# Optimization experiments

Measured on AMD Instinct MI355X. Metric: run time of the kernel, lower is better.

## Reference

```python
import jax, jax.numpy as jnp
import numpy as np

DIM = 512; HEADS = 8; DH = 64; INNER = HEADS * DH
GAMMA = 0.01; LREG = 1e-3
QB = 16; NS = 512


def _ln(x, g, b):
    mu = x.mean(-1, keepdims=True)
    var = jnp.var(x, axis=-1, keepdims=True)  # biased, matches torch LayerNorm
    return (x - mu) / jnp.sqrt(var + 1e-5) * g + b


def _std(x):
    return jnp.std(x, ddof=1)  # torch.std default is unbiased


def setup_inputs() -> dict:
    key = jax.random.key(0)
    ks = jax.random.split(key, 10)
    sc = lambda k, shape: (jax.random.normal(k, shape, jnp.float32) * 0.05)
    return {
        "q": jax.random.normal(ks[0], (QB, NS, DIM), jnp.float32),
        "k": jax.random.normal(ks[1], (QB, NS, DIM), jnp.float32),
        "v": jax.random.normal(ks[2], (QB, NS, DIM), jnp.float32),
        "ln1_g": jnp.ones((DIM,), jnp.float32),
        "ln1_b": jnp.zeros((DIM,), jnp.float32),
        "W_in": sc(ks[3], (DIM, INNER)),
        "wp_w1": sc(ks[4], (2 * DH, 2 * DH)),
        "wp_b1": jnp.zeros((2 * DH,), jnp.float32),
        "wp_ln_g": jnp.ones((2 * DH,), jnp.float32),
        "wp_ln_b": jnp.zeros((2 * DH,), jnp.float32),
        "wp_w2": sc(ks[5], (2 * DH, DH)),
        "wp_b2": jnp.zeros((DH,), jnp.float32),
        "wp_w3": sc(ks[6], (DH, 3)),
        "wp_b3": jnp.zeros((3,), jnp.float32),
        "weight_temp": jnp.array([0.5], jnp.float32),
        "W_out": sc(ks[7], (INNER, DIM)),
        "b_out": jnp.zeros((DIM,), jnp.float32),
    }


def _forward(q, k, v, ln1_g, ln1_b, W_in, wp_w1, wp_b1, wp_ln_g, wp_ln_b,
             wp_w2, wp_b2, wp_w3, wp_b3, weight_temp, W_out, b_out):
    eps = 1e-6

    def proj(t):  # LayerNorm -> Linear(no bias) -> [h, q, n, d]
        y = _ln(t, ln1_g, ln1_b) @ W_in
        Qb, Nb, _ = y.shape
        return y.reshape(Qb, Nb, HEADS, DH).transpose(2, 0, 1, 3)

    f_q, f_k, f_v = proj(q), proj(k), proj(v)
    m = f_k.shape[2]

    # --- cosine distance component ---
    dots_raw = jnp.einsum('hqnd,hqmd->hqnm', f_q, f_k)
    n1 = jnp.linalg.norm(f_q, axis=-1, keepdims=True) + eps          # [h,q,n,1]
    n2 = jnp.linalg.norm(f_k, axis=-1)[:, :, None, :] + eps          # [h,q,1,m]
    cosine_sim = jnp.clip(dots_raw / (n1 * n2), -0.9, 0.9)

    # --- regularized covariance component ---
    fkc = f_k - f_k.mean(axis=2, keepdims=True)   # center keys over n
    fqc = f_q - f_q.mean(axis=-1, keepdims=True)  # center queries over d
    cov = jnp.einsum('hqnd,hqmd->hqnm', fqc, fkc) / (DH ** 0.5 + 1e-6)
    cov = jnp.clip((LREG / max(m, 1)) * cov, -10.0, 10.0)

    # --- margin-based variance component (eval: adaptive_gamma = gamma) ---
    fqn = f_q / jnp.maximum(jnp.linalg.norm(f_q, axis=-1, keepdims=True), 1e-6)
    fkn = f_k / jnp.maximum(jnp.linalg.norm(f_k, axis=-1, keepdims=True), 1e-6)
    cs = jnp.clip(jnp.einsum('hqnd,hqmd->hqnm', fqn, fkn), -0.9, 0.9)
    margin = jnp.clip(GAMMA - cs, 0.0, 5.0)
    var_comp = jnp.broadcast_to(margin.mean(-1, keepdims=True), cs.shape)

    # --- dynamic per-head mixture weights ---
    feat = jnp.concatenate([f_q.mean((1, 2)), f_k.mean((1, 2))], axis=-1)  # [h, 2d]
    x = jax.nn.relu(_ln(feat @ wp_w1 + wp_b1, wp_ln_g, wp_ln_b))
    x = jax.nn.relu(x @ wp_w2 + wp_b2)
    wlog = jax.nn.softmax(x @ wp_w3 + wp_b3, axis=-1)  # predictor ends in Softmax
    wt = jnp.clip(weight_temp, 0.1, 2.0)
    w = jax.nn.softmax(wlog / wt, axis=-1)             # second softmax over temp
    w = jnp.clip(w, 0.05, 0.8)
    w = w / w.sum(-1, keepdims=True)
    cos_w = w[:, 0].reshape(HEADS, 1, 1, 1)
    cov_w = w[:, 1].reshape(HEADS, 1, 1, 1)
    var_w = w[:, 2].reshape(HEADS, 1, 1, 1)

    sg = jax.lax.stop_gradient  # norms are .detach()'d in torch
    dots = (cos_w * (cosine_sim / (sg(_std(cosine_sim)) + 1e-6))
            + cov_w * (cov / (sg(_std(cov)) + 1e-6) * 0.5)
            + var_w * (var_comp / (sg(_std(var_comp)) + 1e-6) * 0.5))

    ds = _std(dots)
    temp = jnp.where(ds < 1e-4, jnp.float32(0.1),
                     jnp.where(ds < 0.01, jnp.float32(0.3), 0.5 + ds))
    temp = jnp.clip(temp, 0.1, 3.0)

    attn = jax.nn.softmax(dots / temp, axis=-1)
    out = jnp.einsum('hqnm,hqmd->hqnd', attn, f_v)
    out = out.transpose(1, 2, 0, 3).reshape(q.shape[0], q.shape[1], INNER)
    return out @ W_out + b_out


def reference(q, k, v, ln1_g, ln1_b, W_in, wp_w1, wp_b1, wp_ln_g, wp_ln_b,
              wp_w2, wp_b2, wp_w3, wp_b3, weight_temp, W_out, b_out):
    return _forward(q, k, v, ln1_g, ln1_b, W_in, wp_w1, wp_b1, wp_ln_g,
                    wp_ln_b, wp_w2, wp_b2, wp_w3, wp_b3, weight_temp,
                    W_out, b_out)
```

## Files before the change

### kernel.cpp

```cpp
#include <hip/hip_runtime.h>
#include <math.h>

#define H 8
#define NS 512
#define D 64

typedef __bf16 bf16x8 __attribute__((ext_vector_type(8)));
typedef float f32x4 __attribute__((ext_vector_type(4)));
typedef short s16x8 __attribute__((ext_vector_type(8)));
typedef short s16x4 __attribute__((ext_vector_type(4)));

#define CS2 ((1e-3f/512.f)/(8.f+1e-6f))
#define LOG2E 1.4426950408889634

static __device__ __forceinline__ f32x4 mfma16(bf16x8 a, bf16x8 b, f32x4 c){
  return __builtin_amdgcn_mfma_f32_16x16x32_bf16(a,b,c,0,0,0);
}
static __device__ __forceinline__ float b2f(unsigned short s){
  union { unsigned u; float f; } v; v.u = ((unsigned)s)<<16; return v.f;
}
static __device__ __forceinline__ unsigned short f2b(float f){
  union { float f; unsigned u; } v; v.f = f;
  unsigned r = v.u + 0x7FFFu + ((v.u>>16)&1u);
  return (unsigned short)(r>>16);
}
static __device__ __forceinline__ float wred64(float v){
  #pragma unroll
  for(int m=32; m>0; m>>=1) v += __shfl_xor(v, m, 64);
  return v;
}

constexpr size_t OFF_XNB = 0;
constexpr size_t OFF_FQB = 6291456;
constexpr size_t OFF_FKB = 8388608;
constexpr size_t OFF_FVB = 10485760;
constexpr size_t OFF_FVT = 12582912;
constexpr size_t OFF_WT  = 14680064;
constexpr size_t OFF_WOH = 14811136;
constexpr size_t OFF_WOL = 14942208;
constexpr size_t OFF_OHH = 15073280;
constexpr size_t OFF_OHL = 17170432;
constexpr size_t OFF_ARR = 19267584;
constexpr size_t OFF_MKB = OFF_ARR + 9*65536;
constexpr size_t OFF_SMK = OFF_MKB + 8192;
constexpr size_t OFF_COEF= OFF_SMK + 128;
constexpr size_t OFF_DBL = OFF_COEF + 32;
constexpr size_t NDBL    = 72 + 1024;

__global__ __launch_bounds__(256) void k_tw(const float* __restrict__ W, unsigned short* __restrict__ WT,
    double* __restrict__ dbl){
  int bx = blockIdx.x; int kt = bx>>3, nt = bx&7;
  int t = threadIdx.x;
  if(bx==0){
    for(int i=t;i<(int)NDBL;i+=256) dbl[i]=0.0;
  }
  __shared__ float tile[64][65];
  #pragma unroll
  for(int i=0;i<4;i++){
    int row = (t>>4) + i*16; int col = (t&15)*4;
    float4 v = *(const float4*)(W + (size_t)(kt*64+row)*512 + nt*64 + col);
    tile[row][col]=v.x; tile[row][col+1]=v.y; tile[row][col+2]=v.z; tile[row][col+3]=v.w;
  }
  __syncthreads();
  #pragma unroll
  for(int i=0;i<4;i++){
    int n = (t>>4) + i*16; int ck = (t&15)*4;
    s16x4 o;
    #pragma unroll
    for(int j=0;j<4;j++) o[j] = (short)f2b(tile[ck+j][n]);
    *(s16x4*)(WT + (size_t)(nt*64+n)*512 + kt*64 + ck) = o;
  }
}

__global__ __launch_bounds__(256) void k_two(const float* __restrict__ W,
    unsigned short* __restrict__ WTh, unsigned short* __restrict__ WTl){
  int bx = blockIdx.x; int kt = bx>>3, nt = bx&7;
  __shared__ float tile[64][65];
  int t = threadIdx.x;
  #pragma unroll
  for(int i=0;i<4;i++){
    int row = (t>>4) + i*16; int col = (t&15)*4;
    float4 v = *(const float4*)(W + (size_t)(kt*64+row)*512 + nt*64 + col);
    tile[row][col]=v.x; tile[row][col+1]=v.y; tile[row][col+2]=v.z; tile[row][col+3]=v.w;
  }
  __syncthreads();
  #pragma unroll
  for(int i=0;i<4;i++){
    int n = (t>>4) + i*16; int ck = (t&15)*4;
    s16x4 oh_, ol_;
    #pragma unroll
    for(int j=0;j<4;j++){
      float x = tile[ck+j][n];
      unsigned short hi = f2b(x);
      oh_[j] = (short)hi;
      ol_[j] = (short)f2b(x - b2f(hi));
    }
    *(s16x4*)(WTh + (size_t)(nt*64+n)*512 + kt*64 + ck) = oh_;
    *(s16x4*)(WTl + (size_t)(nt*64+n)*512 + kt*64 + ck) = ol_;
  }
}

__global__ __launch_bounds__(256) void k_ln(const float* __restrict__ q,
    const float* __restrict__ k, const float* __restrict__ v,
    const float* __restrict__ g, const float* __restrict__ b,
    unsigned short* __restrict__ xnb){
  int row = blockIdx.x*4 + (threadIdx.x>>6); int t = threadIdx.x & 63;
  const float* src = (row < 8192) ? q : ((row < 16384) ? k : v);
  int r = row & 8191;
  const float4* sp = (const float4*)(src + (size_t)r*512);
  float4 v1 = sp[t*2], v2 = sp[t*2+1];
  float s  = v1.x+v1.y+v1.z+v1.w + v2.x+v2.y+v2.z+v2.w;
  float ss = v1.x*v1.x+v1.y*v1.y+v1.z*v1.z+v1.w*v1.w
           + v2.x*v2.x+v2.y*v2.y+v2.z*v2.z+v2.w*v2.w;
  s = wred64(s); ss = wred64(ss);
  float mu = s*(1.f/512.f);
  float var = ss*(1.f/512.f) - mu*mu;
  float rstd = rsqrtf(var + 1e-5f);
  const float4* gp = (const float4*)g; const float4* bp = (const float4*)b;
  float4 g1 = gp[t*2], g2 = gp[t*2+1], b1 = bp[t*2], b2 = bp[t*2+1];
  s16x8 o;
  o[0]=(short)f2b((v1.x-mu)*rstd*g1.x+b1.x); o[1]=(short)f2b((v1.y-mu)*rstd*g1.y+b1.y);
  o[2]=(short)f2b((v1.z-mu)*rstd*g1.z+b1.z); o[3]=(short)f2b((v1.w-mu)*rstd*g1.w+b1.w);
  o[4]=(short)f2b((v2.x-mu)*rstd*g2.x+b2.x); o[5]=(short)f2b((v2.y-mu)*rstd*g2.y+b2.y);
  o[6]=(short)f2b((v2.z-mu)*rstd*g2.z+b2.z); o[7]=(short)f2b((v2.w-mu)*rstd*g2.w+b2.w);
  *(s16x8*)(xnb + (size_t)row*512 + t*8) = o;
}

__global__ __launch_bounds__(256) void k_mm1(const unsigned short* __restrict__ xnb,
    const unsigned short* __restrict__ WT,
    unsigned short* __restrict__ fqb, unsigned short* __restrict__ fkb,
    unsigned short* __restrict__ fvb){
  __shared__ __align__(16) unsigned short As[128*64];
  __shared__ __align__(16) unsigned short Bs[128*64];
  int t = threadIdx.x; int w = t>>6; int l = t&63; int g = l>>4, lc = l&15;
  int Rb = blockIdx.x*128, cb = blockIdx.y*128;
  int wr = (w>>1)*64, wc = (w&1)*64;
  f32x4 acc[4][4];
  #pragma unroll
  for(int i=0;i<4;i++)
    #pragma unroll
    for(int j=0;j<4;j++) acc[i][j] = (f32x4){0.f,0.f,0.f,0.f};
  for(int k0=0; k0<512; k0+=64){
    __syncthreads();
    #pragma unroll
    for(int i=0;i<4;i++){
      int c = t + i*256; int row = c>>3, k8 = c&7;
      s16x8 va = *(const s16x8*)(xnb + (size_t)(Rb+row)*512 + k0 + k8*8);
      *(s16x8*)((char*)As + row*128 + ((k8*16) ^ ((row&7)<<4))) = va;
      s16x8 vb = *(const s16x8*)(WT + (size_t)(cb+row)*512 + k0 + k8*8);
      *(s16x8*)((char*)Bs + row*128 + ((k8*16) ^ ((row&7)<<4))) = vb;
    }
    __syncthreads();
    #pragma unroll
    for(int ks=0; ks<2; ks++){
      bf16x8 ar[4], br[4];
      #pragma unroll
      for(int rt=0; rt<4; rt++){
        int row = wr + rt*16 + lc;
        ar[rt] = *(const bf16x8*)((const char*)As + row*128 + (((ks*4+g)*16) ^ ((row&7)<<4)));
      }
      #pragma unroll
      for(int ct=0; ct<4; ct++){
        int row = wc + ct*16 + lc;
        br[ct] = *(const bf16x8*)((const char*)Bs + row*128 + (((ks*4+g)*16) ^ ((row&7)<<4)));
      }
      #pragma unroll
      for(int rt=0; rt<4; rt++)
        #pragma unroll
        for(int ct=0; ct<4; ct++)
          acc[rt][ct] = mfma16(ar[rt], br[ct], acc[rt][ct]);
    }
  }
  #pragma unroll
  for(int rt=0; rt<4; rt++){
    #pragma unroll
    for(int r=0; r<4; r++){
      int R = Rb + wr + rt*16 + g*4 + r;
      int tsel = R>>13; int rr = R&8191;
      unsigned short* dst = (tsel==0)?fqb:((tsel==1)?fkb:fvb);
      #pragma unroll
      for(int ct=0; ct<4; ct++){
        int c = cb + wc + ct*16 + lc;
        dst[(size_t)rr*512 + c] = f2b(acc[rt][ct][r]);
      }
    }
  }
}

__global__ __launch_bounds__(1024) void k_colstats(const unsigned short* __restrict__ fqb,
    const unsigned short* __restrict__ fkb,
    float* __restrict__ mkb, float* __restrict__ smk, double* featd){
  int hq = blockIdx.x; int h = hq>>4, q = hq&15;
  int t = threadIdx.x; int d = t&63; int g = t>>6;
  __shared__ float cq[16][64], ck[16][64];
  float aq=0.f, ak=0.f;
  for(int n=g; n<512; n+=16){
    size_t base = (size_t)(q*512+n)*512 + h*64 + d;
    aq += b2f(fqb[base]);
    ak += b2f(fkb[base]);
  }
  cq[g][d]=aq; ck[g][d]=ak;
  __syncthreads();
  if(t<64){
    float sq=0.f, sk2=0.f;
    #pragma unroll
    for(int i=0;i<16;i++){ sq+=cq[i][t]; sk2+=ck[i][t]; }
    atomicAdd(&featd[h*128+t], (double)sq);
    atomicAdd(&featd[h*128+64+t], (double)sk2);
    float mk = sk2*(1.f/512.f);
    mkb[hq*64+t]=mk;
    cq[0][t]=mk;
  }
  __syncthreads();
  if(t<64){
    float s = wred64(cq[0][t]);
    if(t==0) smk[hq]=s;
  }
}

__global__ __launch_bounds__(256) void k_rowstats(const unsigned short* __restrict__ fqb,
    const unsigned short* __restrict__ fkb, const float* __restrict__ mkb,
    const float* __restrict__ smk,
    float* __restrict__ ri1, float* __restrict__ mq,
    float* __restrict__ qdm, float* __restrict__ ri2,
    float* __restrict__ sk){
  int b = blockIdx.x; int hq = b>>1; int h = hq>>4, q = hq&15;
  int n = (b&1)*256 + threadIdx.x;
  __shared__ float mk[64];
  if(threadIdx.x<64) mk[threadIdx.x] = mkb[hq*64+threadIdx.x];
  __syncthreads();
  float smkv = smk[hq];
  const unsigned short* fr = fqb + (size_t)(q*512+n)*512 + h*64;
  const unsigned short* kr = fkb + (size_t)(q*512+n)*512 + h*64;
  float sq=0.f, ssq=0.f, dq=0.f, sks=0.f, ssk=0.f;
  #pragma unroll
  for(int j=0;j<8;j++){
    s16x8 vq = *(const s16x8*)(fr + j*8);
    s16x8 vk = *(const s16x8*)(kr + j*8);
    #pragma unroll
    for(int e=0;e<8;e++){
      float a = b2f((unsigned short)vq[e]);
      float c = b2f((unsigned short)vk[e]);
      sq += a; ssq += a*a; dq += a*mk[j*8+e];
      sks += c; ssk += c*c;
    }
  }
  int idx = hq*512 + n;
  float nq = sqrtf(ssq);
  ri1[idx]  = 1.f/(nq+1e-6f);
  mq[idx]   = sq*(1.f/64.f);
  qdm[idx]  = dq;
  float nk = sqrtf(ssk);
  ri2[idx]  = 1.f/(nk+1e-6f);
  sk[idx]   = sks - smkv;
}

__global__ __launch_bounds__(256) void k_vt(const unsigned short* __restrict__ fvb,
    unsigned short* __restrict__ fvT){
  int bx = blockIdx.x; int hq = bx>>2, nc = bx&3;
  int h = hq>>4, q = hq&15; int n0 = nc*128;
  __shared__ float tile[128][65];
  int t = threadIdx.x;
  #pragma unroll
  for(int i=0;i<4;i++){
    int c = t + i*256; int row = c>>3, k8 = c&7;
    s16x8 v = *(const s16x8*)(fvb + (size_t)(q*512 + n0 + row)*512 + h*64 + k8*8);
    #pragma unroll
    for(int j=0;j<8;j++) tile[row][k8*8+j] = b2f((unsigned short)v[j]);
  }
  __syncthreads();
  #pragma unroll
  for(int i=0;i<4;i++){
    int c = t + i*256; int d = c>>4, n8 = c&15;
    s16x8 o;
    #pragma unroll
    for(int j=0;j<8;j++){
      int p = n8*8+j;
      int pl = p & 31;
      int src = (p & ~31) | (16*(pl&1) + (pl>>1));
      o[j] = (short)f2b(tile[src][d]);
    }
    *(s16x8*)(fvT + (size_t)(hq*64 + d)*512 + n0 + n8*8) = o;
  }
}

__global__ __launch_bounds__(256) void k_comp(const unsigned short* __restrict__ fqb,
    const unsigned short* __restrict__ fkb,
    const float* __restrict__ ri1,
    const float* __restrict__ mq, const float* __restrict__ qdm,
    const float* __restrict__ ri2,
    const float* __restrict__ skp,
    float* __restrict__ mxcg, float* __restrict__ mxvg, double* headsum){
  int bx = blockIdx.x; int hq = bx>>3; int rt = bx&7;
  int h = hq>>4, q = hq&15; int n0 = rt*64;
  __shared__ __align__(16) unsigned short Qs[64*64];
  __shared__ __align__(16) unsigned short Ks[128*64];
  __shared__ float ri2f[512], skf[512];
  __shared__ float red[4][9];
  int t = threadIdx.x; int w = t>>6; int l = t&63; int g = l>>4, lc = l&15;
  for(int i=t; i<512; i+=256){
    ri2f[i]=ri2[hq*NS+i]; skf[i]=skp[hq*NS+i];
  }
  #pragma unroll
  for(int i=0;i<2;i++){
    int c = t + i*256; int row = c>>3, k8 = c&7;
    s16x8 v = *(const s16x8*)(fqb + (size_t)(q*512 + n0 + row)*512 + h*64 + k8*8);
    *(s16x8*)((char*)Qs + row*128 + ((k8*16) ^ ((row&7)<<4))) = v;
  }
  float ri1r[4], mqr[4], qdmr[4];
  #pragma unroll
  for(int r=0;r<4;r++){
    int n = hq*NS + n0 + w*16 + g*4 + r;
    ri1r[r]=ri1[n]; mqr[r]=mq[n]; qdmr[r]=qdm[n];
  }
  __syncthreads();
  bf16x8 aq[2];
  #pragma unroll
  for(int ks=0;ks<2;ks++){
    int row = 16*w + lc;
    aq[ks] = *(const bf16x8*)((const char*)Qs + row*128 + (((ks*4+g)*16) ^ ((row&7)<<4)));
  }
  float p1=0,p3=0,p4=0;
  float rm_m[4]={0,0,0,0}, rm_c[4]={0,0,0,0}, rm_v[4]={0,0,0,0};
  float mxc[4]={-1e30f,-1e30f,-1e30f,-1e30f}, mxv[4]={-1e30f,-1e30f,-1e30f,-1e30f};
  for(int mc=0; mc<4; mc++){
    __syncthreads();
    #pragma unroll
    for(int i=0;i<4;i++){
      int c = t + i*256; int row = c>>3, k8 = c&7;
      s16x8 v = *(const s16x8*)(fkb + (size_t)(q*512 + mc*128 + row)*512 + h*64 + k8*8);
      *(s16x8*)((char*)Ks + row*128 + ((k8*16) ^ ((row&7)<<4))) = v;
    }
    __syncthreads();
    #pragma unroll 2
    for(int mt=0; mt<8; mt++){
      f32x4 dacc = (f32x4){0.f,0.f,0.f,0.f};
      #pragma unroll
      for(int ks=0;ks<2;ks++){
        int row = mt*16 + lc;
        bf16x8 bk = *(const bf16x8*)((const char*)Ks + row*128 + (((ks*4+g)*16) ^ ((row&7)<<4)));
        dacc = mfma16(aq[ks], bk, dacc);
      }
      int m = mc*128 + mt*16 + lc;
      float r2 = ri2f[m], sc = skf[m];
      #pragma unroll
      for(int r=0;r<4;r++){
        float dv = dacc[r];
        float cosv = fminf(fmaxf(dv*ri1r[r]*r2, -0.9f), 0.9f);
        float inner = (dv - qdmr[r]) - mqr[r]*sc;
        float marg = fmaxf(0.01f - cosv, 0.f);
        p1 += cosv*cosv; p3 += inner*inner; p4 += cosv*inner;
        rm_m[r]+=marg; rm_c[r]+=cosv; rm_v[r]+=inner;
        mxc[r]=fmaxf(mxc[r],cosv); mxv[r]=fmaxf(mxv[r],inner);
      }
    }
  }
  float p0 = rm_c[0]+rm_c[1]+rm_c[2]+rm_c[3];
  float p2 = rm_v[0]+rm_v[1]+rm_v[2]+rm_v[3];
  #pragma unroll
  for(int off=1; off<16; off<<=1){
    #pragma unroll
    for(int r=0;r<4;r++){
      rm_m[r]+=__shfl_xor(rm_m[r],off,64);
      rm_c[r]+=__shfl_xor(rm_c[r],off,64);
      rm_v[r]+=__shfl_xor(rm_v[r],off,64);
      mxc[r]=fmaxf(mxc[r],__shfl_xor(mxc[r],off,64));
      mxv[r]=fmaxf(mxv[r],__shfl_xor(mxv[r],off,64));
    }
  }
  float q0=0,q1=0,q2=0,q3=0;
  if(lc==0){
    #pragma unroll
    for(int r=0;r<4;r++){
      float vmv = rm_m[r]*(1.f/512.f);
      q0+=vmv; q1+=vmv*vmv; q2+=vmv*rm_c[r]; q3+=vmv*rm_v[r];
      int n = n0 + w*16 + g*4 + r;
      mxcg[hq*NS+n]=mxc[r]; mxvg[hq*NS+n]=mxv[r];
    }
  }
  float all9[9] = {p0,p1,p2,p3,p4,q0,q1,q2,q3};
  #pragma unroll
  for(int j=0;j<9;j++){
    float vv = wred64(all9[j]);
    if(l==0) red[w][j]=vv;
  }
  __syncthreads();
  if(t<9){
    double s = (double)red[0][t]+(double)red[1][t]+(double)red[2][t]+(double)red[3][t];
    atomicAdd(&headsum[h*9+t], s);
  }
}

__global__ __launch_bounds__(1024) void k_finalize(const double* headsum, const double* featd,
    const float* __restrict__ w1, const float* __restrict__ b1,
    const float* __restrict__ lng, const float* __restrict__ lnb,
    const float* __restrict__ w2, const float* __restrict__ b2,
    const float* __restrict__ w3, const float* __restrict__ b3,
    const float* __restrict__ wtemp, float* coef){
  __shared__ float featS[8][128];
  __shared__ float x1S[8][128];
  __shared__ float x2S[8][64];
  __shared__ float redS[8][4];
  __shared__ float oS[8][3];
  __shared__ float whS[8][3];
  int t = threadIdx.x;
  int h = t>>7, j = t&127;
  featS[h][j] = (float)(featd[t] * (1.0/8192.0));
  __syncthreads();
  float a = 0.f;
  #pragma unroll 16
  for(int i=0;i<128;i++) a += featS[h][i]*w1[(size_t)i*128+j];
  a += b1[j];
  {
    float s = a, ss = a*a;
    #pragma unroll
    for(int m=32;m>0;m>>=1){ s += __shfl_xor(s,m,64); ss += __shfl_xor(ss,m,64); }
    int wv = (t>>6)&1;
    if((t&63)==0){ redS[h][wv*2]=s; redS[h][wv*2+1]=ss; }
  }
  __syncthreads();
  {
    float sum = redS[h][0]+redS[h][2], sumsq = redS[h][1]+redS[h][3];
    float mu = sum*(1.f/128.f);
    float var = sumsq*(1.f/128.f)-mu*mu;
    float rstd = rsqrtf(var+1e-5f);
    x1S[h][j] = fmaxf((a-mu)*rstd*lng[j]+lnb[j], 0.f);
  }
  __syncthreads();
  if(t < 512){
    int h2 = t>>6, j2 = t&63;
    float s2 = 0.f;
    #pragma unroll 16
    for(int i=0;i<128;i++) s2 += x1S[h2][i]*w2[(size_t)i*64+j2];
    x2S[h2][j2] = fmaxf(s2+b2[j2], 0.f);
  }
  __syncthreads();
  if(t < 24){
    int h3 = t/3, j3 = t-h3*3;
    float s3=0.f;
    #pragma unroll 16
    for(int i=0;i<64;i++) s3 += x2S[h3][i]*w3[i*3+j3];
    oS[h3][j3] = s3 + b3[j3];
  }
  __syncthreads();
  if(t < 8){
    float o0=oS[t][0], o1=oS[t][1], o2=oS[t][2];
    float mx=fmaxf(o0,fmaxf(o1,o2));
    float e0=expf(o0-mx), e1=expf(o1-mx), e2=expf(o2-mx), se=e0+e1+e2;
    float l0=e0/se, l1=e1/se, l2=e2/se;
    float wt=fminf(fmaxf(wtemp[0],0.1f),2.0f);
    l0/=wt; l1/=wt; l2/=wt;
    mx=fmaxf(l0,fmaxf(l1,l2));
    e0=expf(l0-mx); e1=expf(l1-mx); e2=expf(l2-mx); se=e0+e1+e2;
    float u0=fminf(fmaxf(e0/se,0.05f),0.8f);
    float u1=fminf(fmaxf(e1/se,0.05f),0.8f);
    float u2=fminf(fmaxf(e2/se,0.05f),0.8f);
    float su=u0+u1+u2;
    whS[t][0]=u0/su; whS[t][1]=u1/su; whS[t][2]=u2/su;
  }
  __syncthreads();
  if(t==0){
    const double N = 33554432.0;
    const double CS2d = (double)CS2;
    double gs[9];
    for(int jj=0;jj<9;jj++){ double s=0; for(int hh=0;hh<8;hh++) s+=headsum[hh*9+jj]; gs[jj]=s; }
    auto sd = [&](double s, double ss)->double{
      double v=(ss - s*s/N)/(N-1.0); return v>0.0 ? sqrt(v) : 0.0;
    };
    double std_cos = sd(gs[0],gs[1]);
    double std_cov = sd(CS2d*gs[2], CS2d*CS2d*gs[3]);
    double std_vm  = sd(512.0*gs[5], 512.0*gs[6]);
    double sdot=0.0, sdot2=0.0;
    double Af[8], Bf[8];
    for(int hh=0;hh<8;hh++){
      const double* hs = headsum + hh*9;
      double A = (double)whS[hh][0]/(std_cos+1e-6);
      double Bi = (double)whS[hh][1]/(std_cov+1e-6)*0.5*CS2d;
      double C = (double)whS[hh][2]/(std_vm +1e-6)*0.5;
      sdot  += A*hs[0] + Bi*hs[2] + C*512.0*hs[5];
      sdot2 += A*A*hs[1] + Bi*Bi*hs[3] + C*C*512.0*hs[6]
             + 2.0*A*Bi*hs[4] + 2.0*A*C*hs[7] + 2.0*Bi*C*hs[8];
      Af[hh]=A; Bf[hh]=Bi;
    }
    double dstd = sd(sdot, sdot2);
    double temp = dstd < 1e-4 ? 0.1 : (dstd < 0.01 ? 0.3 : 0.5 + dstd);
    temp = fmin(fmax(temp, 0.1), 3.0);
    for(int hh=0;hh<8;hh++){
      coef[hh]   = (float)(Af[hh]/temp*LOG2E);
      coef[8+hh] = (float)(Bf[hh]/temp*LOG2E);
    }
    coef[16] = (float)temp;
  }
}

__global__ __launch_bounds__(256) void k_flash(const unsigned short* __restrict__ fqb,
    const unsigned short* __restrict__ fkb, const unsigned short* __restrict__ fvT,
    const float* __restrict__ ri1, const float* __restrict__ mq,
    const float* __restrict__ qdm, const float* __restrict__ ri2,
    const float* __restrict__ skp,
    const float* __restrict__ mxcg, const float* __restrict__ mxvg,
    const float* __restrict__ coef,
    unsigned short* __restrict__ ohh, unsigned short* __restrict__ ohl){
  int bx = blockIdx.x; int hq = bx>>3; int rt = bx&7;
  int h = hq>>4, q = hq&15; int n0 = rt*64;
  __shared__ __align__(16) unsigned short Qs[64*64];
  __shared__ __align__(16) unsigned short Ks[128*64];
  __shared__ __align__(16) unsigned short Vt[64*128];
  __shared__ __align__(16) unsigned short Ps[4][16*40];
  __shared__ float ri2f[512], skf[512];
  int t = threadIdx.x; int w = t>>6; int l = t&63; int g = l>>4, lc = l&15;
  for(int i=t; i<512; i+=256){ ri2f[i]=ri2[hq*NS+i]; skf[i]=skp[hq*NS+i]; }
  #pragma unroll
  for(int i=0;i<2;i++){
    int c = t + i*256; int row = c>>3, k8 = c&7;
    s16x8 v = *(const s16x8*)(fqb + (size_t)(q*512 + n0 + row)*512 + h*64 + k8*8);
    *(s16x8*)((char*)Qs + row*128 + ((k8*16) ^ ((row&7)<<4))) = v;
  }
  float Ah = coef[h], Bh = coef[8+h];
  float ri1r[4], mqr[4], qdmr[4], Mr[4];
  #pragma unroll
  for(int r=0;r<4;r++){
    int n = hq*NS + n0 + w*16 + g*4 + r;
    ri1r[r]=ri1[n]; mqr[r]=mq[n]; qdmr[r]=qdm[n];
    Mr[r] = Ah*mxcg[n] + Bh*mxvg[n];
  }
  __syncthreads();
  bf16x8 aq[2];
  #pragma unroll
  for(int ks=0;ks<2;ks++){
    int row = 16*w + lc;
    aq[ks] = *(const bf16x8*)((const char*)Qs + row*128 + (((ks*4+g)*16) ^ ((row&7)<<4)));
  }
  f32x4 acc[4];
  #pragma unroll
  for(int dt=0;dt<4;dt++) acc[dt] = (f32x4){0.f,0.f,0.f,0.f};
  float lsum[4]={0.f,0.f,0.f,0.f};
  unsigned short* Pw = &Ps[w][0];
  unsigned* Pu = (unsigned*)Pw;
  for(int mc=0; mc<4; mc++){
    __syncthreads();
    #pragma unroll
    for(int i=0;i<4;i++){
      int c = t + i*256; int row = c>>3, k8 = c&7;
      s16x8 v = *(const s16x8*)(fkb + (size_t)(q*512 + mc*128 + row)*512 + h*64 + k8*8);
      *(s16x8*)((char*)Ks + row*128 + ((k8*16) ^ ((row&7)<<4))) = v;
    }
    #pragma unroll
    for(int i=0;i<4;i++){
      int c = t + i*256; int d = c>>4, m8 = c&15;
      s16x8 v = *(const s16x8*)(fvT + (size_t)(hq*64 + d)*512 + mc*128 + m8*8);
      *(s16x8*)((char*)Vt + d*256 + ((m8*16) ^ ((d&7)<<4))) = v;
    }
    __syncthreads();
    #pragma unroll 1
    for(int mt2=0; mt2<4; mt2++){
      f32x4 d0 = (f32x4){0.f,0.f,0.f,0.f};
      f32x4 d1 = (f32x4){0.f,0.f,0.f,0.f};
      #pragma unroll
      for(int ks=0;ks<2;ks++){
        int row0 = (mt2*2)*16 + lc;
        bf16x8 bk0 = *(const bf16x8*)((const char*)Ks + row0*128 + (((ks*4+g)*16) ^ ((row0&7)<<4)));
        d0 = mfma16(aq[ks], bk0, d0);
        int row1 = (mt2*2+1)*16 + lc;
        bf16x8 bk1 = *(const bf16x8*)((const char*)Ks + row1*128 + (((ks*4+g)*16) ^ ((row1&7)<<4)));
        d1 = mfma16(aq[ks], bk1, d1);
      }
      int m0 = mc*128 + mt2*32 + lc;
      float r20 = ri2f[m0],    sc0 = skf[m0];
      float r21 = ri2f[m0+16], sc1 = skf[m0+16];
      #pragma unroll
      for(int r=0;r<4;r++){
        float dv0 = d0[r], dv1 = d1[r];
        float c0 = fminf(fmaxf(dv0*ri1r[r]*r20, -0.9f), 0.9f);
        float c1 = fminf(fmaxf(dv1*ri1r[r]*r21, -0.9f), 0.9f);
        float i0 = (dv0 - qdmr[r]) - mqr[r]*sc0;
        float i1 = (dv1 - qdmr[r]) - mqr[r]*sc1;
        float pe0 = __builtin_amdgcn_exp2f(fmaxf(Ah*c0 + Bh*i0 - Mr[r], -120.f));
        float pe1 = __builtin_amdgcn_exp2f(fmaxf(Ah*c1 + Bh*i1 - Mr[r], -120.f));
        lsum[r] += pe0 + pe1;
        unsigned pk = ((unsigned)f2b(pe1) << 16) | (unsigned)f2b(pe0);
        Pu[(g*4+r)*20 + lc] = pk;
      }
      asm volatile("s_waitcnt lgkmcnt(0)" ::: "memory");
      bf16x8 ap = *(const bf16x8*)((const char*)Pw + lc*80 + g*16);
      #pragma unroll
      for(int dt=0;dt<4;dt++){
        int drow = dt*16 + lc;
        bf16x8 bv = *(const bf16x8*)((const char*)Vt + drow*256 + (((mt2*4+g)*16) ^ ((drow&7)<<4)));
        acc[dt] = mfma16(ap, bv, acc[dt]);
      }
    }
  }
  #pragma unroll
  for(int off=1; off<16; off<<=1){
    #pragma unroll
    for(int r=0;r<4;r++) lsum[r] += __shfl_xor(lsum[r], off, 64);
  }
  #pragma unroll
  for(int r=0;r<4;r++){
    float inv = 1.f/lsum[r];
    int n = n0 + w*16 + g*4 + r;
    #pragma unroll
    for(int dt=0;dt<4;dt++){
      size_t idx = (size_t)(q*512 + n)*512 + h*64 + dt*16 + lc;
      float val = acc[dt][r]*inv;
      unsigned short hi = f2b(val);
      ohh[idx] = hi;
      ohl[idx] = f2b(val - b2f(hi));
    }
  }
}

__global__ __launch_bounds__(256) void k_gout2(const unsigned short* __restrict__ Ahp,
    const unsigned short* __restrict__ Alp,
    const unsigned short* __restrict__ Bhp, const unsigned short* __restrict__ Blp,
    const float* __restrict__ bias, float* __restrict__ Cout){
  __shared__ __align__(16) unsigned short AsH[128*64];
  __shared__ __align__(16) unsigned short AsL[128*64];
  __shared__ __align__(16) unsigned short BsH[128*64];
  __shared__ __align__(16) unsigned short BsL[128*64];
  int t = threadIdx.x; int w = t>>6; int l = t&63; int g = l>>4, lc = l&15;
  int Rb = blockIdx.x*128, cb = blockIdx.y*128;
  int wr = (w>>1)*64, wc = (w&1)*64;
  f32x4 acc[4][4];
  #pragma unroll
  for(int i=0;i<4;i++)
    #pragma unroll
    for(int j=0;j<4;j++) acc[i][j] = (f32x4){0.f,0.f,0.f,0.f};
  for(int k0=0; k0<512; k0+=64){
    __syncthreads();
    #pragma unroll
    for(int i=0;i<4;i++){
      int c = t + i*256; int row = c>>3, k8 = c&7;
      int sw = (k8*16) ^ ((row&7)<<4);
      *(s16x8*)((char*)AsH + row*128 + sw) = *(const s16x8*)(Ahp + (size_t)(Rb+row)*512 + k0 + k8*8);
      *(s16x8*)((char*)AsL + row*128 + sw) = *(const s16x8*)(Alp + (size_t)(Rb+row)*512 + k0 + k8*8);
      *(s16x8*)((char*)BsH + row*128 + sw) = *(const s16x8*)(Bhp + (size_t)(cb+row)*512 + k0 + k8*8);
      *(s16x8*)((char*)BsL + row*128 + sw) = *(const s16x8*)(Blp + (size_t)(cb+row)*512 + k0 + k8*8);
    }
    __syncthreads();
    #pragma unroll
    for(int ks=0; ks<2; ks++){
      bf16x8 arh[4], arl[4], brh[4], brl[4];
      #pragma unroll
      for(int rt=0; rt<4; rt++){
        int row = wr + rt*16 + lc;
        int off = row*128 + (((ks*4+g)*16) ^ ((row&7)<<4));
        arh[rt] = *(const bf16x8*)((const char*)AsH + off);
        arl[rt] = *(const bf16x8*)((const char*)AsL + off);
      }
      #pragma unroll
      for(int ct=0; ct<4; ct++){
        int row = wc + ct*16 + lc;
        int off = row*128 + (((ks*4+g)*16) ^ ((row&7)<<4));
        brh[ct] = *(const bf16x8*)((const char*)BsH + off);
        brl[ct] = *(const bf16x8*)((const char*)BsL + off);
      }
      #pragma unroll
      for(int rt=0; rt<4; rt++)
        #pragma unroll
        for(int ct=0; ct<4; ct++){
          acc[rt][ct] = mfma16(arh[rt], brh[ct], acc[rt][ct]);
          acc[rt][ct] = mfma16(arh[rt], brl[ct], acc[rt][ct]);
          acc[rt][ct] = mfma16(arl[rt], brh[ct], acc[rt][ct]);
        }
    }
  }
  #pragma unroll
  for(int rt=0; rt<4; rt++){
    #pragma unroll
    for(int r=0; r<4; r++){
      int R = Rb + wr + rt*16 + g*4 + r;
      #pragma unroll
      for(int ct=0; ct<4; ct++){
        int c = cb + wc + ct*16 + lc;
        Cout[(size_t)R*512 + c] = acc[rt][ct][r] + bias[c];
      }
    }
  }
}

extern "C" void kernel_launch(void* const* d_in, const int* in_sizes, int n_in,
                              void* d_out, int out_size, void* d_ws, size_t ws_size,
                              hipStream_t stream){
  const float* q    = (const float*)d_in[0];
  const float* k    = (const float*)d_in[1];
  const float* v    = (const float*)d_in[2];
  const float* ln1g = (const float*)d_in[3];
  const float* ln1b = (const float*)d_in[4];
  const float* Win  = (const float*)d_in[5];
  const float* w1   = (const float*)d_in[6];
  const float* b1   = (const float*)d_in[7];
  const float* lng  = (const float*)d_in[8];
  const float* lnb  = (const float*)d_in[9];
  const float* w2   = (const float*)d_in[10];
  const float* b2   = (const float*)d_in[11];
  const float* w3   = (const float*)d_in[12];
  const float* b3   = (const float*)d_in[13];
  const float* wtemp= (const float*)d_in[14];
  const float* Wout = (const float*)d_in[15];
  const float* bout = (const float*)d_in[16];

  float* w = (float*)d_ws;
  unsigned short* xnb = (unsigned short*)(w + OFF_XNB);
  unsigned short* fqb = (unsigned short*)(w + OFF_FQB);
  unsigned short* fkb = (unsigned short*)(w + OFF_FKB);
  unsigned short* fvb = (unsigned short*)(w + OFF_FVB);
  unsigned short* fvT = (unsigned short*)(w + OFF_FVT);
  unsigned short* wtb = (unsigned short*)(w + OFF_WT);
  unsigned short* woh = (unsigned short*)(w + OFF_WOH);
  unsigned short* wol = (unsigned short*)(w + OFF_WOL);
  unsigned short* ohh = (unsigned short*)(w + OFF_OHH);
  unsigned short* ohl = (unsigned short*)(w + OFF_OHL);
  float* ri1  = w + OFF_ARR + 0*65536;
  float* mq_  = w + OFF_ARR + 2*65536;
  float* qdm  = w + OFF_ARR + 3*65536;
  float* ri2  = w + OFF_ARR + 4*65536;
  float* sk_  = w + OFF_ARR + 6*65536;
  float* mxc  = w + OFF_ARR + 7*65536;
  float* mxv  = w + OFF_ARR + 8*65536;
  float* mkb  = w + OFF_MKB;
  float* smk_ = w + OFF_SMK;
  float* coef = w + OFF_COEF;
  double* dbl = (double*)(w + OFF_DBL);
  double* headsum = dbl;
  double* featd   = dbl + 72;

  k_tw<<<64, 256, 0, stream>>>(Win, wtb, dbl);
  k_two<<<64, 256, 0, stream>>>(Wout, woh, wol);
  k_ln<<<6144, 256, 0, stream>>>(q, k, v, ln1g, ln1b, xnb);
  k_mm1<<<dim3(192,4), 256, 0, stream>>>(xnb, wtb, fqb, fkb, fvb);
  k_colstats<<<128, 1024, 0, stream>>>(fqb, fkb, mkb, smk_, featd);
  k_rowstats<<<256, 256, 0, stream>>>(fqb, fkb, mkb, smk_, ri1, mq_, qdm, ri2, sk_);
  k_vt<<<512, 256, 0, stream>>>(fvb, fvT);
  k_comp<<<1024, 256, 0, stream>>>(fqb, fkb, ri1, mq_, qdm, ri2, sk_, mxc, mxv, headsum);
  k_finalize<<<1, 1024, 0, stream>>>(headsum, featd, w1, b1, lng, lnb, w2, b2, w3, b3, wtemp, coef);
  k_flash<<<1024, 256, 0, stream>>>(fqb, fkb, fvT, ri1, mq_, qdm, ri2, sk_, mxc, mxv, coef, ohh, ohl);
  k_gout2<<<dim3(64,4), 256, 0, stream>>>(ohh, ohl, woh, wol, bout, (float*)d_out);
}
```

Measured before the change: 168.6 us.

## Merge prep kernels, fuse stats and V transpose, use fp16 P·V in flash

Merges the weight-transpose and LayerNorm launches into one grid, and folds the column stats, row stats and V transpose into a single launch. This cuts the launch count from 11 to 7. In the flash kernel, the exponent arithmetic is refactored into precomputed per-row FMA constants and the -120 clamp is dropped. The P matrix and transposed V now use fp16 with packed RTZ conversion and an f16 MFMA instead of a manual bf16 round. The P scratch buffer reuses the Q shared-memory tile to save LDS, which relies on Q already being in registers. Without the clamp, underflow of fp16 P may change accuracy slightly.

```diff
diff --git a/kernel.cpp b/kernel.cpp
--- a/kernel.cpp
+++ b/kernel.cpp
@@ -6,6 +6,7 @@
 #define D 64
 
 typedef __bf16 bf16x8 __attribute__((ext_vector_type(8)));
+typedef _Float16 f16x8 __attribute__((ext_vector_type(8)));
 typedef float f32x4 __attribute__((ext_vector_type(4)));
 typedef short s16x8 __attribute__((ext_vector_type(8)));
 typedef short s16x4 __attribute__((ext_vector_type(4)));
@@ -15,6 +16,9 @@
 
 static __device__ __forceinline__ f32x4 mfma16(bf16x8 a, bf16x8 b, f32x4 c){
   return __builtin_amdgcn_mfma_f32_16x16x32_bf16(a,b,c,0,0,0);
+}
+static __device__ __forceinline__ f32x4 mfma16h(f16x8 a, f16x8 b, f32x4 c){
+  return __builtin_amdgcn_mfma_f32_16x16x32_f16(a,b,c,0,0,0);
 }
 static __device__ __forceinline__ float b2f(unsigned short s){
   union { unsigned u; float f; } v; v.u = ((unsigned)s)<<16; return v.f;
@@ -47,83 +51,82 @@
 constexpr size_t OFF_DBL = OFF_COEF + 32;
 constexpr size_t NDBL    = 72 + 1024;
 
-__global__ __launch_bounds__(256) void k_tw(const float* __restrict__ W, unsigned short* __restrict__ WT,
-    double* __restrict__ dbl){
-  int bx = blockIdx.x; int kt = bx>>3, nt = bx&7;
-  int t = threadIdx.x;
-  if(bx==0){
-    for(int i=t;i<(int)NDBL;i+=256) dbl[i]=0.0;
-  }
-  __shared__ float tile[64][65];
-  #pragma unroll
-  for(int i=0;i<4;i++){
-    int row = (t>>4) + i*16; int col = (t&15)*4;
-    float4 v = *(const float4*)(W + (size_t)(kt*64+row)*512 + nt*64 + col);
-    tile[row][col]=v.x; tile[row][col+1]=v.y; tile[row][col+2]=v.z; tile[row][col+3]=v.w;
-  }
-  __syncthreads();
-  #pragma unroll
-  for(int i=0;i<4;i++){
-    int n = (t>>4) + i*16; int ck = (t&15)*4;
-    s16x4 o;
-    #pragma unroll
-    for(int j=0;j<4;j++) o[j] = (short)f2b(tile[ck+j][n]);
-    *(s16x4*)(WT + (size_t)(nt*64+n)*512 + kt*64 + ck) = o;
-  }
-}
-
-__global__ __launch_bounds__(256) void k_two(const float* __restrict__ W,
-    unsigned short* __restrict__ WTh, unsigned short* __restrict__ WTl){
-  int bx = blockIdx.x; int kt = bx>>3, nt = bx&7;
-  __shared__ float tile[64][65];
-  int t = threadIdx.x;
-  #pragma unroll
-  for(int i=0;i<4;i++){
-    int row = (t>>4) + i*16; int col = (t&15)*4;
-    float4 v = *(const float4*)(W + (size_t)(kt*64+row)*512 + nt*64 + col);
-    tile[row][col]=v.x; tile[row][col+1]=v.y; tile[row][col+2]=v.z; tile[row][col+3]=v.w;
-  }
-  __syncthreads();
-  #pragma unroll
-  for(int i=0;i<4;i++){
-    int n = (t>>4) + i*16; int ck = (t&15)*4;
-    s16x4 oh_, ol_;
-    #pragma unroll
-    for(int j=0;j<4;j++){
-      float x = tile[ck+j][n];
-      unsigned short hi = f2b(x);
-      oh_[j] = (short)hi;
-      ol_[j] = (short)f2b(x - b2f(hi));
-    }
-    *(s16x4*)(WTh + (size_t)(nt*64+n)*512 + kt*64 + ck) = oh_;
-    *(s16x4*)(WTl + (size_t)(nt*64+n)*512 + kt*64 + ck) = ol_;
-  }
-}
-
-__global__ __launch_bounds__(256) void k_ln(const float* __restrict__ q,
+__global__ __launch_bounds__(256) void k_pre(const float* __restrict__ q,
     const float* __restrict__ k, const float* __restrict__ v,
     const float* __restrict__ g, const float* __restrict__ b,
-    unsigned short* __restrict__ xnb){
-  int row = blockIdx.x*4 + (threadIdx.x>>6); int t = threadIdx.x & 63;
-  const float* src = (row < 8192) ? q : ((row < 16384) ? k : v);
-  int r = row & 8191;
-  const float4* sp = (const float4*)(src + (size_t)r*512);
-  float4 v1 = sp[t*2], v2 = sp[t*2+1];
-  float s  = v1.x+v1.y+v1.z+v1.w + v2.x+v2.y+v2.z+v2.w;
-  float ss = v1.x*v1.x+v1.y*v1.y+v1.z*v1.z+v1.w*v1.w
-           + v2.x*v2.x+v2.y*v2.y+v2.z*v2.z+v2.w*v2.w;
-  s = wred64(s); ss = wred64(ss);
-  float mu = s*(1.f/512.f);
-  float var = ss*(1.f/512.f) - mu*mu;
-  float rstd = rsqrtf(var + 1e-5f);
-  const float4* gp = (const float4*)g; const float4* bp = (const float4*)b;
-  float4 g1 = gp[t*2], g2 = gp[t*2+1], b1 = bp[t*2], b2 = bp[t*2+1];
-  s16x8 o;
-  o[0]=(short)f2b((v1.x-mu)*rstd*g1.x+b1.x); o[1]=(short)f2b((v1.y-mu)*rstd*g1.y+b1.y);
-  o[2]=(short)f2b((v1.z-mu)*rstd*g1.z+b1.z); o[3]=(short)f2b((v1.w-mu)*rstd*g1.w+b1.w);
-  o[4]=(short)f2b((v2.x-mu)*rstd*g2.x+b2.x); o[5]=(short)f2b((v2.y-mu)*rstd*g2.y+b2.y);
-  o[6]=(short)f2b((v2.z-mu)*rstd*g2.z+b2.z); o[7]=(short)f2b((v2.w-mu)*rstd*g2.w+b2.w);
-  *(s16x8*)(xnb + (size_t)row*512 + t*8) = o;
+    const float* __restrict__ Win, const float* __restrict__ Wout,
+    unsigned short* __restrict__ xnb, unsigned short* __restrict__ WT,
+    unsigned short* __restrict__ WTh, unsigned short* __restrict__ WTl,
+    double* __restrict__ dbl){
+  int bx = blockIdx.x; int t = threadIdx.x;
+  if(bx < 6144){
+    int row = bx*4 + (t>>6); int l = t & 63;
+    const float* src = (row < 8192) ? q : ((row < 16384) ? k : v);
+    int r = row & 8191;
+    const float4* sp = (const float4*)(src + (size_t)r*512);
+    float4 v1 = sp[l*2], v2 = sp[l*2+1];
+    float s  = v1.x+v1.y+v1.z+v1.w + v2.x+v2.y+v2.z+v2.w;
+    float ss = v1.x*v1.x+v1.y*v1.y+v1.z*v1.z+v1.w*v1.w
+             + v2.x*v2.x+v2.y*v2.y+v2.z*v2.z+v2.w*v2.w;
+    s = wred64(s); ss = wred64(ss);
+    float mu = s*(1.f/512.f);
+    float var = ss*(1.f/512.f) - mu*mu;
+    float rstd = rsqrtf(var + 1e-5f);
+    const float4* gp = (const float4*)g; const float4* bp = (const float4*)b;
+    float4 g1 = gp[l*2], g2 = gp[l*2+1], b1 = bp[l*2], b2 = bp[l*2+1];
+    s16x8 o;
+    o[0]=(short)f2b((v1.x-mu)*rstd*g1.x+b1.x); o[1]=(short)f2b((v1.y-mu)*rstd*g1.y+b1.y);
+    o[2]=(short)f2b((v1.z-mu)*rstd*g1.z+b1.z); o[3]=(short)f2b((v1.w-mu)*rstd*g1.w+b1.w);
+    o[4]=(short)f2b((v2.x-mu)*rstd*g2.x+b2.x); o[5]=(short)f2b((v2.y-mu)*rstd*g2.y+b2.y);
+    o[6]=(short)f2b((v2.z-mu)*rstd*g2.z+b2.z); o[7]=(short)f2b((v2.w-mu)*rstd*g2.w+b2.w);
+    *(s16x8*)(xnb + (size_t)row*512 + l*8) = o;
+    return;
+  }
+  __shared__ float tile[64][65];
+  if(bx < 6208){
+    int bb = bx - 6144; int kt = bb>>3, nt = bb&7;
+    if(bb==0){
+      for(int i=t;i<(int)NDBL;i+=256) dbl[i]=0.0;
+    }
+    #pragma unroll
+    for(int i=0;i<4;i++){
+      int row = (t>>4) + i*16; int col = (t&15)*4;
+      float4 vv = *(const float4*)(Win + (size_t)(kt*64+row)*512 + nt*64 + col);
+      tile[row][col]=vv.x; tile[row][col+1]=vv.y; tile[row][col+2]=vv.z; tile[row][col+3]=vv.w;
+    }
+    __syncthreads();
+    #pragma unroll
+    for(int i=0;i<4;i++){
+      int n = (t>>4) + i*16; int ck = (t&15)*4;
+      s16x4 o;
+      #pragma unroll
+      for(int j=0;j<4;j++) o[j] = (short)f2b(tile[ck+j][n]);
+      *(s16x4*)(WT + (size_t)(nt*64+n)*512 + kt*64 + ck) = o;
+    }
+  } else {
+    int bb = bx - 6208; int kt = bb>>3, nt = bb&7;
+    #pragma unroll
+    for(int i=0;i<4;i++){
+      int row = (t>>4) + i*16; int col = (t&15)*4;
+      float4 vv = *(const float4*)(Wout + (size_t)(kt*64+row)*512 + nt*64 + col);
+      tile[row][col]=vv.x; tile[row][col+1]=vv.y; tile[row][col+2]=vv.z; tile[row][col+3]=vv.w;
+    }
+    __syncthreads();
+    #pragma unroll
+    for(int i=0;i<4;i++){
+      int n = (t>>4) + i*16; int ck = (t&15)*4;
+      s16x4 oh_, ol_;
+      #pragma unroll
+      for(int j=0;j<4;j++){
+        float x = tile[ck+j][n];
+        unsigned short hi = f2b(x);
+        oh_[j] = (short)hi;
+        ol_[j] = (short)f2b(x - b2f(hi));
+      }
+      *(s16x4*)(WTh + (size_t)(nt*64+n)*512 + kt*64 + ck) = oh_;
+      *(s16x4*)(WTl + (size_t)(nt*64+n)*512 + kt*64 + ck) = ol_;
+    }
+  }
 }
 
 __global__ __launch_bounds__(256) void k_mm1(const unsigned short* __restrict__ xnb,
@@ -187,100 +190,95 @@
   }
 }
 
-__global__ __launch_bounds__(1024) void k_colstats(const unsigned short* __restrict__ fqb,
-    const unsigned short* __restrict__ fkb,
-    float* __restrict__ mkb, float* __restrict__ smk, double* featd){
-  int hq = blockIdx.x; int h = hq>>4, q = hq&15;
-  int t = threadIdx.x; int d = t&63; int g = t>>6;
-  __shared__ float cq[16][64], ck[16][64];
-  float aq=0.f, ak=0.f;
-  for(int n=g; n<512; n+=16){
-    size_t base = (size_t)(q*512+n)*512 + h*64 + d;
-    aq += b2f(fqb[base]);
-    ak += b2f(fkb[base]);
-  }
-  cq[g][d]=aq; ck[g][d]=ak;
-  __syncthreads();
-  if(t<64){
-    float sq=0.f, sk2=0.f;
-    #pragma unroll
-    for(int i=0;i<16;i++){ sq+=cq[i][t]; sk2+=ck[i][t]; }
-    atomicAdd(&featd[h*128+t], (double)sq);
-    atomicAdd(&featd[h*128+64+t], (double)sk2);
-    float mk = sk2*(1.f/512.f);
-    mkb[hq*64+t]=mk;
-    cq[0][t]=mk;
-  }
-  __syncthreads();
-  if(t<64){
-    float s = wred64(cq[0][t]);
-    if(t==0) smk[hq]=s;
-  }
-}
-
-__global__ __launch_bounds__(256) void k_rowstats(const unsigned short* __restrict__ fqb,
-    const unsigned short* __restrict__ fkb, const float* __restrict__ mkb,
-    const float* __restrict__ smk,
-    float* __restrict__ ri1, float* __restrict__ mq,
-    float* __restrict__ qdm, float* __restrict__ ri2,
-    float* __restrict__ sk){
-  int b = blockIdx.x; int hq = b>>1; int h = hq>>4, q = hq&15;
-  int n = (b&1)*256 + threadIdx.x;
-  __shared__ float mk[64];
-  if(threadIdx.x<64) mk[threadIdx.x] = mkb[hq*64+threadIdx.x];
-  __syncthreads();
-  float smkv = smk[hq];
-  const unsigned short* fr = fqb + (size_t)(q*512+n)*512 + h*64;
-  const unsigned short* kr = fkb + (size_t)(q*512+n)*512 + h*64;
-  float sq=0.f, ssq=0.f, dq=0.f, sks=0.f, ssk=0.f;
-  #pragma unroll
-  for(int j=0;j<8;j++){
-    s16x8 vq = *(const s16x8*)(fr + j*8);
-    s16x8 vk = *(const s16x8*)(kr + j*8);
-    #pragma unroll
-    for(int e=0;e<8;e++){
-      float a = b2f((unsigned short)vq[e]);
-      float c = b2f((unsigned short)vk[e]);
-      sq += a; ssq += a*a; dq += a*mk[j*8+e];
-      sks += c; ssk += c*c;
-    }
-  }
-  int idx = hq*512 + n;
-  float nq = sqrtf(ssq);
-  ri1[idx]  = 1.f/(nq+1e-6f);
-  mq[idx]   = sq*(1.f/64.f);
-  qdm[idx]  = dq;
-  float nk = sqrtf(ssk);
-  ri2[idx]  = 1.f/(nk+1e-6f);
-  sk[idx]   = sks - smkv;
-}
-
-__global__ __launch_bounds__(256) void k_vt(const unsigned short* __restrict__ fvb,
+__global__ __launch_bounds__(512) void k_mid(const unsigned short* __restrict__ fqb,
+    const unsigned short* __restrict__ fkb, const unsigned short* __restrict__ fvb,
+    float* __restrict__ mkb, float* __restrict__ smk, double* featd,
+    float* __restrict__ ri1, float* __restrict__ mq, float* __restrict__ qdm,
+    float* __restrict__ ri2, float* __restrict__ sk,
     unsigned short* __restrict__ fvT){
-  int bx = blockIdx.x; int hq = bx>>2, nc = bx&3;
-  int h = hq>>4, q = hq&15; int n0 = nc*128;
-  __shared__ float tile[128][65];
-  int t = threadIdx.x;
-  #pragma unroll
-  for(int i=0;i<4;i++){
-    int c = t + i*256; int row = c>>3, k8 = c&7;
-    s16x8 v = *(const s16x8*)(fvb + (size_t)(q*512 + n0 + row)*512 + h*64 + k8*8);
-    #pragma unroll
-    for(int j=0;j<8;j++) tile[row][k8*8+j] = b2f((unsigned short)v[j]);
-  }
-  __syncthreads();
-  #pragma unroll
-  for(int i=0;i<4;i++){
-    int c = t + i*256; int d = c>>4, n8 = c&15;
-    s16x8 o;
-    #pragma unroll
-    for(int j=0;j<8;j++){
-      int p = n8*8+j;
-      int pl = p & 31;
-      int src = (p & ~31) | (16*(pl&1) + (pl>>1));
-      o[j] = (short)f2b(tile[src][d]);
-    }
-    *(s16x8*)(fvT + (size_t)(hq*64 + d)*512 + n0 + n8*8) = o;
+  int bx = blockIdx.x; int t = threadIdx.x;
+  if(bx < 128){
+    int hq = bx; int h = hq>>4, q = hq&15;
+    __shared__ float cq[8][64], ck[8][64], mkS[64];
+    __shared__ float smkS;
+    {
+      int d = t&63; int g = t>>6;
+      float aq=0.f, ak=0.f;
+      for(int n=g; n<512; n+=8){
+        size_t base = (size_t)(q*512+n)*512 + h*64 + d;
+        aq += b2f(fqb[base]);
+        ak += b2f(fkb[base]);
+      }
+      cq[g][d]=aq; ck[g][d]=ak;
+    }
+    __syncthreads();
+    if(t<64){
+      float sq=0.f, sk2=0.f;
+      #pragma unroll
+      for(int i=0;i<8;i++){ sq+=cq[i][t]; sk2+=ck[i][t]; }
+      atomicAdd(&featd[h*128+t], (double)sq);
+      atomicAdd(&featd[h*128+64+t], (double)sk2);
+      float mk = sk2*(1.f/512.f);
+      mkb[hq*64+t]=mk; mkS[t]=mk;
+      float s = wred64(mk);
+      if(t==0){ smk[hq]=s; smkS=s; }
+    }
+    __syncthreads();
+    {
+      int n = t;
+      float smkv = smkS;
+      const unsigned short* fr = fqb + (size_t)(q*512+n)*512 + h*64;
+      const unsigned short* kr = fkb + (size_t)(q*512+n)*512 + h*64;
+      float sq=0.f, ssq=0.f, dq=0.f, sks=0.f, ssk=0.f;
+      #pragma unroll
+      for(int j=0;j<8;j++){
+        s16x8 vq = *(const s16x8*)(fr + j*8);
+        s16x8 vk = *(const s16x8*)(kr + j*8);
+        #pragma unroll
+        for(int e=0;e<8;e++){
+          float a = b2f((unsigned short)vq[e]);
+          float c = b2f((unsigned short)vk[e]);
+          sq += a; ssq += a*a; dq += a*mkS[j*8+e];
+          sks += c; ssk += c*c;
+        }
+      }
+      int idx = hq*512 + n;
+      float nq = sqrtf(ssq);
+      ri1[idx]  = 1.f/(nq+1e-6f);
+      mq[idx]   = sq*(1.f/64.f);
+      qdm[idx]  = dq;
+      float nk = sqrtf(ssk);
+      ri2[idx]  = 1.f/(nk+1e-6f);
+      sk[idx]   = sks - smkv;
+    }
+    return;
+  }
+  {
+    int bb = bx - 128; int hq = bb>>2, nc = bb&3;
+    int h = hq>>4, q = hq&15; int n0 = nc*128;
+    __shared__ float tile[128][65];
+    #pragma unroll
+    for(int i=0;i<2;i++){
+      int c = t + i*512; int row = c>>3, k8 = c&7;
+      s16x8 v = *(const s16x8*)(fvb + (size_t)(q*512 + n0 + row)*512 + h*64 + k8*8);
+      #pragma unroll
+      for(int j=0;j<8;j++) tile[row][k8*8+j] = b2f((unsigned short)v[j]);
+    }
+    __syncthreads();
+    #pragma unroll
+    for(int i=0;i<2;i++){
+      int c = t + i*512; int d = c>>4, n8 = c&15;
+      s16x8 o;
+      #pragma unroll
+      for(int j=0;j<8;j++){
+        int p = n8*8+j;
+        int pl = p & 31;
+        int src = (p & ~31) | (16*(pl&1) + (pl>>1));
+        union { _Float16 hl; short s; } cv; cv.hl = (_Float16)tile[src][d];
+        o[j] = cv.s;
+      }
+      *(s16x8*)(fvT + (size_t)(hq*64 + d)*512 + n0 + n8*8) = o;
+    }
   }
 }
 
@@ -506,7 +504,6 @@
   __shared__ __align__(16) unsigned short Qs[64*64];
   __shared__ __align__(16) unsigned short Ks[128*64];
   __shared__ __align__(16) unsigned short Vt[64*128];
-  __shared__ __align__(16) unsigned short Ps[4][16*40];
   __shared__ float ri2f[512], skf[512];
   int t = threadIdx.x; int w = t>>6; int l = t&63; int g = l>>4, lc = l&15;
   for(int i=t; i<512; i+=256){ ri2f[i]=ri2[hq*NS+i]; skf[i]=skp[hq*NS+i]; }
@@ -517,12 +514,15 @@
     *(s16x8*)((char*)Qs + row*128 + ((k8*16) ^ ((row&7)<<4))) = v;
   }
   float Ah = coef[h], Bh = coef[8+h];
-  float ri1r[4], mqr[4], qdmr[4], Mr[4];
+  float loA = -0.9f*Ah, hiA = 0.9f*Ah;
+  float ri1A[4], R1[4], R2[4];
   #pragma unroll
   for(int r=0;r<4;r++){
     int n = hq*NS + n0 + w*16 + g*4 + r;
-    ri1r[r]=ri1[n]; mqr[r]=mq[n]; qdmr[r]=qdm[n];
-    Mr[r] = Ah*mxcg[n] + Bh*mxvg[n];
+    float Mr = Ah*mxcg[n] + Bh*mxvg[n];
+    ri1A[r] = ri1[n]*Ah;
+    R1[r] = fmaf(Bh, qdm[n], Mr);
+    R2[r] = Bh*mq[n];
   }
   __syncthreads();
   bf16x8 aq[2];
@@ -535,7 +535,7 @@
   #pragma unroll
   for(int dt=0;dt<4;dt++) acc[dt] = (f32x4){0.f,0.f,0.f,0.f};
   float lsum[4]={0.f,0.f,0.f,0.f};
-  unsigned short* Pw = &Ps[w][0];
+  unsigned short* Pw = Qs + w*640;
   unsigned* Pu = (unsigned*)Pw;
   for(int mc=0; mc<4; mc++){
     __syncthreads();
@@ -571,23 +571,24 @@
       #pragma unroll
       for(int r=0;r<4;r++){
         float dv0 = d0[r], dv1 = d1[r];
-        float c0 = fminf(fmaxf(dv0*ri1r[r]*r20, -0.9f), 0.9f);
-        float c1 = fminf(fmaxf(dv1*ri1r[r]*r21, -0.9f), 0.9f);
-        float i0 = (dv0 - qdmr[r]) - mqr[r]*sc0;
-        float i1 = (dv1 - qdmr[r]) - mqr[r]*sc1;
-        float pe0 = __builtin_amdgcn_exp2f(fmaxf(Ah*c0 + Bh*i0 - Mr[r], -120.f));
-        float pe1 = __builtin_amdgcn_exp2f(fmaxf(Ah*c1 + Bh*i1 - Mr[r], -120.f));
+        float cl0 = fminf(fmaxf(dv0*ri1A[r]*r20, loA), hiA);
+        float cl1 = fminf(fmaxf(dv1*ri1A[r]*r21, loA), hiA);
+        float e0 = fmaf(-R2[r], sc0, fmaf(Bh, dv0, -R1[r]));
+        float e1 = fmaf(-R2[r], sc1, fmaf(Bh, dv1, -R1[r]));
+        float pe0 = __builtin_amdgcn_exp2f(cl0 + e0);
+        float pe1 = __builtin_amdgcn_exp2f(cl1 + e1);
         lsum[r] += pe0 + pe1;
-        unsigned pk = ((unsigned)f2b(pe1) << 16) | (unsigned)f2b(pe0);
+        auto ph = __builtin_amdgcn_cvt_pkrtz(pe0, pe1);
+        unsigned pk; __builtin_memcpy(&pk, &ph, 4);
         Pu[(g*4+r)*20 + lc] = pk;
       }
       asm volatile("s_waitcnt lgkmcnt(0)" ::: "memory");
-      bf16x8 ap = *(const bf16x8*)((const char*)Pw + lc*80 + g*16);
+      f16x8 ap = *(const f16x8*)((const char*)Pw + lc*80 + g*16);
       #pragma unroll
       for(int dt=0;dt<4;dt++){
         int drow = dt*16 + lc;
-        bf16x8 bv = *(const bf16x8*)((const char*)Vt + drow*256 + (((mt2*4+g)*16) ^ ((drow&7)<<4)));
-        acc[dt] = mfma16(ap, bv, acc[dt]);
+        f16x8 bv = *(const f16x8*)((const char*)Vt + drow*256 + (((mt2*4+g)*16) ^ ((drow&7)<<4)));
+        acc[dt] = mfma16h(ap, bv, acc[dt]);
       }
     }
   }
@@ -726,13 +727,9 @@
   double* headsum = dbl;
   double* featd   = dbl + 72;
 
-  k_tw<<<64, 256, 0, stream>>>(Win, wtb, dbl);
-  k_two<<<64, 256, 0, stream>>>(Wout, woh, wol);
-  k_ln<<<6144, 256, 0, stream>>>(q, k, v, ln1g, ln1b, xnb);
+  k_pre<<<6272, 256, 0, stream>>>(q, k, v, ln1g, ln1b, Win, Wout, xnb, wtb, woh, wol, dbl);
   k_mm1<<<dim3(192,4), 256, 0, stream>>>(xnb, wtb, fqb, fkb, fvb);
-  k_colstats<<<128, 1024, 0, stream>>>(fqb, fkb, mkb, smk_, featd);
-  k_rowstats<<<256, 256, 0, stream>>>(fqb, fkb, mkb, smk_, ri1, mq_, qdm, ri2, sk_);
-  k_vt<<<512, 256, 0, stream>>>(fvb, fvT);
+  k_mid<<<640, 512, 0, stream>>>(fqb, fkb, fvb, mkb, smk_, featd, ri1, mq_, qdm, ri2, sk_, fvT);
   k_comp<<<1024, 256, 0, stream>>>(fqb, fkb, ri1, mq_, qdm, ri2, sk_, mxc, mxv, headsum);
   k_finalize<<<1, 1024, 0, stream>>>(headsum, featd, w1, b1, lng, lnb, w2, b2, w3, b3, wtemp, coef);
   k_flash<<<1024, 256, 0, stream>>>(fqb, fkb, fvT, ri1, mq_, qdm, ri2, sk_, mxc, mxv, coef, ohh, ohl);
```

Measured after the change: 159.2 us. 5.5% less time.
